# Kernel optimization log

Hardware: AMD Instinct MI355X
Metric: run time of the kernel (lower is better)

## Reference

```python
import jax, jax.numpy as jnp
import numpy as np
import math

D_MODEL = 512
N_HEADS = 8
D_HEAD = D_MODEL // N_HEADS
TEMP = math.sqrt(D_HEAD)


def setup_inputs() -> dict:
    key = jax.random.key(0)
    k1, k2, k3, k4, k5, k6 = jax.random.split(key, 6)
    B, L = 4, 2048
    q = jax.random.normal(k1, (B, L, D_MODEL), dtype=jnp.float32)
    # bool mask, True -> zero out post-softmax attention (matches torch.where branch)
    mask = jax.random.bernoulli(k2, 0.1, (B, L, L))
    in_weight = jax.random.normal(k3, (3 * D_MODEL, D_MODEL), dtype=jnp.float32) * 0.02
    in_bias = jax.random.normal(k4, (3 * D_MODEL,), dtype=jnp.float32) * 0.02
    out_w = jax.random.normal(k5, (D_MODEL, D_MODEL), dtype=jnp.float32) * 0.02
    out_b = jax.random.normal(k6, (D_MODEL,), dtype=jnp.float32) * 0.02
    return {"q": q, "mask": mask, "in_weight": in_weight, "in_bias": in_bias,
            "out_w": out_w, "out_b": out_b}


def reference(q, mask, in_weight, in_bias, out_w, out_b):
    B, L, D = q.shape
    # per-head weight slicing exactly as the torch reshape: (H, E, 3, D)
    W = in_weight.reshape(N_HEADS, D_HEAD, 3, D)
    Bv = in_bias.reshape(N_HEADS, D_HEAD, 3)
    qw, kw, vw = W[:, :, 0, :], W[:, :, 1, :], W[:, :, 2, :]  # (H, E, D)
    qb, kb, vb = Bv[:, :, 0], Bv[:, :, 1], Bv[:, :, 2]        # (H, E)
    # self-attention: k = q, v = q (forward defaults)
    Q = jnp.einsum('bld,hed->bhle', q, qw) + qb[None, :, None, :]
    K = jnp.einsum('bld,hed->bhle', q, kw) + kb[None, :, None, :]
    V = jnp.einsum('bld,hed->bhle', q, vw) + vb[None, :, None, :]
    atn = jax.nn.softmax(jnp.einsum('bhqe,bhke->bhqk', Q, K) / TEMP, axis=-1)
    # post-softmax bool masking (faithful to the original non-standard order)
    atn = jnp.where(mask[:, None, :, :], jnp.zeros((), atn.dtype), atn)
    # QUIRK of source: attention() returns V (not atn @ V); heads = concat of V
    heads = V.transpose(0, 2, 1, 3).reshape(B, L, D)  # (B, L, D_MODEL)
    outputs = heads @ out_w.T + out_b
    masks = atn.sum(axis=1)  # sum over heads -> (B, Lq, Lk)
    return outputs, masks
```

## Files before the change

kernel.cpp:

```cpp
#include <hip/hip_runtime.h>

typedef unsigned short u16;
typedef unsigned int u32;
typedef __bf16 bf16x8 __attribute__((ext_vector_type(8)));
typedef float f32x4 __attribute__((ext_vector_type(4)));

#define B_SZ 4
#define L_SZ 2048
#define D_SZ 512
#define H_SZ 8
#define E_SZ 64

#define Q_SCALE 0.18033688011112042f

#define WS_FLAG   0
#define WS_WPACK  1024
#define WS_BPACK  (WS_WPACK + 1572864)
#define WS_WOUT   (WS_BPACK + 6144)
#define WS_QBF    (WS_WOUT + 524288)
#define WS_Q      (WS_QBF + 8388608)
#define WS_K      (WS_Q + 8388608)
#define WS_V      (WS_K + 8388608)
#define WS_STATS  (WS_V + 8388608)

static __device__ __forceinline__ u16 f2bf(float f) {
  unsigned int u = __float_as_uint(f);
  u += 0x7FFFu + ((u >> 16) & 1u);
  return (u16)(u >> 16);
}

static __device__ __forceinline__ float fexp2(float x) {
  return __builtin_amdgcn_exp2f(x);
}

union FragU { bf16x8 v; uint4 u4; unsigned long long ul[2]; };

static __device__ __forceinline__ int gperm(int d) {
  int t = d & 31;
  return (d & ~31) | ((t & 12) << 1) | ((t & 16) >> 2) | (t & 3);
}

static __device__ __forceinline__ bf16x8 qfrag(const u16* __restrict__ Qp,
                                               int row, int half, int lg) {
  FragU f;
  f.u4 = *reinterpret_cast<const uint4*>(
      (const char*)Qp + (size_t)row * 128 + (half << 6) + (lg << 4));
  return f.v;
}

static __device__ __forceinline__ void gload_lds16(const void* g, void* l) {
  __builtin_amdgcn_global_load_lds(
      (const __attribute__((address_space(1))) void*)g,
      (__attribute__((address_space(3))) void*)l, 16, 0, 0);
}

template<int NT, int NCHUNK>
static __device__ __forceinline__ void stage_ktile(const u16* __restrict__ Kh, int kb0,
                                                   char* tile, int tid) {
  int wbase = (tid & ~63) * 16;
#pragma unroll
  for (int i = 0; i < NCHUNK / NT; i++) {
    int cl = tid + i * NT;
    int r = cl >> 3, c = cl & 7;
    const char* g = (const char*)Kh + (size_t)(kb0 + r) * 128 + ((c ^ (r & 7)) << 4);
    gload_lds16(g, tile + wbase + i * NT * 16);
  }
}

static __device__ __forceinline__ bf16x8 lds_frag(const char* tile, int c, int half,
                                                  int lr, int lg) {
  int r = c * 16 + lr;
  int off = ((half << 6) | (lg << 4)) ^ ((r & 7) << 4);
  FragU f;
  f.u4 = *reinterpret_cast<const uint4*>(tile + r * 128 + off);
  return f.v;
}

__global__ __launch_bounds__(256) void kdetect(const unsigned int* __restrict__ w,
                                               int* __restrict__ flag) {
  int fB = 0, fF = 0;
  for (int i = blockIdx.x * blockDim.x + threadIdx.x; i < 262144;
       i += gridDim.x * blockDim.x) {
    unsigned int v = w[i];
    if (v == 0x3F800000u) fF = 1;
    else if (v > 1u) fB = 1;
  }
  if (__any(fB)) { if ((threadIdx.x & 63) == 0) atomicOr(&flag[0], 1); }
  if (__any(fF)) { if ((threadIdx.x & 63) == 0) atomicOr(&flag[1], 1); }
}

__global__ __launch_bounds__(256) void kcast(const float* __restrict__ q,
                                             u16* __restrict__ qbf) {
  int i = blockIdx.x * blockDim.x + threadIdx.x;
  int row = i >> 6, c = i & 63;
  int g = c >> 2, lg = c & 3;
  const float* src = q + (size_t)row * 512 + g * 32 + lg * 4;
  float4 v0 = *reinterpret_cast<const float4*>(src);
  float4 v1 = *reinterpret_cast<const float4*>(src + 16);
  u32 w0 = f2bf(v0.x) | ((u32)f2bf(v0.y) << 16);
  u32 w1 = f2bf(v0.z) | ((u32)f2bf(v0.w) << 16);
  u32 w2 = f2bf(v1.x) | ((u32)f2bf(v1.y) << 16);
  u32 w3 = f2bf(v1.z) | ((u32)f2bf(v1.w) << 16);
  uint4 out = {w0, w1, w2, w3};
  *reinterpret_cast<uint4*>(qbf + (size_t)row * 512 + c * 8) = out;
}

__global__ __launch_bounds__(256) void kpack(const float* __restrict__ w_in,
                                             const float* __restrict__ b_in,
                                             const float* __restrict__ w_out,
                                             u16* __restrict__ Wpack, float* __restrict__ bpack,
                                             u16* __restrict__ Wout) {
  const int T0 = 1536 * 512;
  const int T1 = T0 + 512 * 512;
  const int T2 = T1 + 1536;
  for (int i = blockIdx.x * blockDim.x + threadIdx.x; i < T2; i += gridDim.x * blockDim.x) {
    if (i < T0) {
      int n = i >> 9, d = i & 511;
      int sel = n >> 9, idx = n & 511;
      int h = idx >> 6, e = idx & 63;
      int row = h * 192 + e * 3 + sel;
      float v = w_in[row * 512 + d];
      if (sel == 0) v *= Q_SCALE;
      Wpack[(size_t)n * 512 + gperm(d)] = f2bf(v);
    } else if (i < T1) {
      int j = i - T0;
      int n = j >> 9, d = j & 511;
      Wout[(size_t)n * 512 + gperm(d)] = f2bf(w_out[j]);
    } else {
      int n = i - T1;
      int sel = n >> 9, idx = n & 511;
      int h = idx >> 6, e = idx & 63;
      int row = h * 192 + e * 3 + sel;
      float v = b_in[row];
      if (sel == 0) v *= Q_SCALE;
      bpack[n] = v;
    }
  }
}

static __device__ __forceinline__ void stage_tile(const u16* __restrict__ A,
                                                  const u16* __restrict__ Bw,
                                                  int m0, int n0, int t,
                                                  char* tA, char* tB, int tid) {
  int w64 = tid & ~63;
#pragma unroll
  for (int i = 0; i < 4; i++) {
    int cl = tid + i * 256;
    int r = cl >> 3, c = cl & 7;
    size_t gofs = (size_t)r * 1024 + t * 128 + ((c ^ (r & 7)) << 4);
    gload_lds16((const char*)A + (size_t)m0 * 1024 + gofs, tA + (i * 256 + w64) * 16);
    gload_lds16((const char*)Bw + (size_t)n0 * 1024 + gofs, tB + (i * 256 + w64) * 16);
  }
}

template<int MODE>
__global__ __launch_bounds__(256) void kgemm(const u16* __restrict__ A,
                                             const u16* __restrict__ Bw,
                                             const float* __restrict__ bias,
                                             u16* __restrict__ Qb, u16* __restrict__ Kb,
                                             u16* __restrict__ Vb, float* __restrict__ outp) {
  __shared__ __align__(128) char tA[2][16384], tB[2][16384];
  int tid = threadIdx.x;
  int w = tid >> 6, lane = tid & 63;
  int lr = lane & 15, lg = lane >> 4;
  int m0 = blockIdx.x * 128, n0 = blockIdx.y * 128;
  int wr = w >> 1, wc = w & 1;

  f32x4 acc[4][4] = {};

  stage_tile(A, Bw, m0, n0, 0, tA[0], tB[0], tid);
  __syncthreads();
#pragma unroll 1
  for (int t = 0; t < 8; t++) {
    if (t < 7) stage_tile(A, Bw, m0, n0, t + 1, tA[(t + 1) & 1], tB[(t + 1) & 1], tid);
    const char* mA = tA[t & 1] + wr * 64 * 128;
    const char* mB = tB[t & 1] + wc * 64 * 128;
#pragma unroll
    for (int gg = 0; gg < 2; gg++) {
      bf16x8 af[4], bf_[4];
#pragma unroll
      for (int i = 0; i < 4; i++) af[i] = lds_frag(mA, i, gg, lr, lg);
#pragma unroll
      for (int j = 0; j < 4; j++) bf_[j] = lds_frag(mB, j, gg, lr, lg);
#pragma unroll
      for (int i = 0; i < 4; i++)
#pragma unroll
        for (int j = 0; j < 4; j++)
          acc[i][j] = __builtin_amdgcn_mfma_f32_16x16x32_bf16(af[i], bf_[j], acc[i][j], 0, 0, 0);
    }
    __syncthreads();
  }

#pragma unroll
  for (int j = 0; j < 4; j++) {
    int col = n0 + wc * 64 + j * 16 + lr;
    float bb = bias[col];
#pragma unroll
    for (int i = 0; i < 4; i++) {
#pragma unroll
      for (int jj = 0; jj < 4; jj++) {
        int row = m0 + wr * 64 + i * 16 + lg * 4 + jj;
        float val = acc[i][j][jj] + bb;
        if (MODE == 1) {
          outp[(size_t)row * 512 + col] = val;
        } else {
          u16 bv = f2bf(val);
          int b = row >> 11, l = row & 2047;
          if (col < 512) {
            int h = col >> 6, e = col & 63;
            Qb[((((size_t)(b * 8 + h)) << 11) + l) * 64 + gperm(e)] = bv;
          } else if (col < 1024) {
            int c2 = col - 512, h = c2 >> 6, e = c2 & 63;
            Kb[((((size_t)(b * 8 + h)) << 11) + l) * 64 + gperm(e)] = bv;
          } else {
            Vb[(size_t)row * 512 + gperm(col - 1024)] = bv;
          }
        }
      }
    }
  }
}

__global__ __launch_bounds__(256, 4) void kstats(const u16* __restrict__ Qb,
                                                 const u16* __restrict__ Kb,
                                                 float* __restrict__ stats) {
  __shared__ __align__(128) char tile[2][8192];
  int bh = blockIdx.x;
  int tid = threadIdx.x;
  int w = tid >> 6, lane = tid & 63;
  int lr = lane & 15, lg = lane >> 4;
  int q0 = blockIdx.y * 64 + w * 16;
  const u16* Qp = Qb + (size_t)bh * L_SZ * E_SZ;
  const u16* Kp = Kb + (size_t)bh * L_SZ * E_SZ;

  bf16x8 bq0 = qfrag(Qp, q0 + lr, 0, lg);
  bf16x8 bq1 = qfrag(Qp, q0 + lr, 1, lg);
  float s0 = 0.0f;

  stage_ktile<256, 512>(Kp, 0, tile[0], tid);
  __syncthreads();
#pragma unroll 1
  for (int t = 0; t < 32; t++) {
    if (t + 1 < 32) stage_ktile<256, 512>(Kp, (t + 1) * 64, tile[(t + 1) & 1], tid);
    const char* tl = tile[t & 1];
#pragma unroll
    for (int c = 0; c < 4; c++) {
      bf16x8 a0 = lds_frag(tl, c, 0, lr, lg);
      bf16x8 a1 = lds_frag(tl, c, 1, lr, lg);
      f32x4 d = {0.f, 0.f, 0.f, 0.f};
      d = __builtin_amdgcn_mfma_f32_16x16x32_bf16(a0, bq0, d, 0, 0, 0);
      d = __builtin_amdgcn_mfma_f32_16x16x32_bf16(a1, bq1, d, 0, 0, 0);
      s0 += fexp2(d[0]) + fexp2(d[1]) + fexp2(d[2]) + fexp2(d[3]);
    }
    __syncthreads();
  }
  s0 += __shfl_xor(s0, 16);
  s0 += __shfl_xor(s0, 32);
  if (lane < 16) stats[(size_t)bh * L_SZ + q0 + lr] = 1.0f / s0;
}

#define KM_PACKMASK(BITS, QOFS)                                                  \
  {                                                                              \
    size_t moff = mb + (size_t)(q0 + (QOFS) + lr) * L_SZ + kb0;                  \
    if (mode == 0) {                                                             \
      _Pragma("unroll")                                                          \
      for (int c = 0; c < 4; c++) {                                              \
        int4 mi = *reinterpret_cast<const int4*>((const int*)mask + moff + c * 16 + lg * 4); \
        BITS |= (mi.x ? 1u : 0u) << (c * 4);                                     \
        BITS |= (mi.y ? 1u : 0u) << (c * 4 + 1);                                 \
        BITS |= (mi.z ? 1u : 0u) << (c * 4 + 2);                                 \
        BITS |= (mi.w ? 1u : 0u) << (c * 4 + 3);                                 \
      }                                                                          \
    } else if (mode == 1) {                                                      \
      _Pragma("unroll")                                                          \
      for (int c = 0; c < 4; c++) {                                              \
        u32 mw = *reinterpret_cast<const u32*>((const unsigned char*)mask + moff + c * 16 + lg * 4); \
        BITS |= ((mw & 0x000000FFu) ? 1u : 0u) << (c * 4);                       \
        BITS |= ((mw & 0x0000FF00u) ? 1u : 0u) << (c * 4 + 1);                   \
        BITS |= ((mw & 0x00FF0000u) ? 1u : 0u) << (c * 4 + 2);                   \
        BITS |= ((mw & 0xFF000000u) ? 1u : 0u) << (c * 4 + 3);                   \
      }                                                                          \
    } else {                                                                     \
      _Pragma("unroll")                                                          \
      for (int c = 0; c < 4; c++) {                                              \
        float4 mf = *reinterpret_cast<const float4*>((const float*)mask + moff + c * 16 + lg * 4); \
        BITS |= ((mf.x != 0.f) ? 1u : 0u) << (c * 4);                            \
        BITS |= ((mf.y != 0.f) ? 1u : 0u) << (c * 4 + 1);                        \
        BITS |= ((mf.z != 0.f) ? 1u : 0u) << (c * 4 + 2);                        \
        BITS |= ((mf.w != 0.f) ? 1u : 0u) << (c * 4 + 3);                        \
      }                                                                          \
    }                                                                            \
  }

#define KM_EPILOGUE(PACC, QOFS, BITS)                                            \
  {                                                                              \
    int q = q0 + (QOFS) + lr;                                                    \
    float* mrow = mbase_out + (size_t)q * L_SZ + kb0;                            \
    _Pragma("unroll")                                                            \
    for (int c = 0; c < 4; c++) {                                                \
      int kk = c * 16 + lg * 4;                                                  \
      f32x4 v = PACC[c];                                                         \
      if ((BITS >> (c * 4 + 0)) & 1u) v[0] = 0.f;                                \
      if ((BITS >> (c * 4 + 1)) & 1u) v[1] = 0.f;                                \
      if ((BITS >> (c * 4 + 2)) & 1u) v[2] = 0.f;                                \
      if ((BITS >> (c * 4 + 3)) & 1u) v[3] = 0.f;                                \
      *reinterpret_cast<f32x4*>(mrow + kk) = v;                                  \
    }                                                                            \
  }

__global__ __launch_bounds__(256, 4) void kmasks(const u16* __restrict__ Qb,
                                                 const u16* __restrict__ Kb,
                                                 const float* __restrict__ stats,
                                                 const void* __restrict__ mask,
                                                 const int* __restrict__ flag,
                                                 float* __restrict__ outp) {
  __shared__ __align__(128) char tile[2][8192];
  int b = blockIdx.z;
  int tid = threadIdx.x;
  int w = tid >> 6, lane = tid & 63;
  int lr = lane & 15, lg = lane >> 4;
  int q0 = blockIdx.y * 128 + w * 32;
  int kb0 = blockIdx.x * 64;
  int mode = flag[0] ? 1 : (flag[1] ? 2 : 0);
  const size_t LE = (size_t)L_SZ * E_SZ;
  size_t mb = (size_t)b * L_SZ * L_SZ;

  f32x4 P0[4] = {}, P1[4] = {};

  stage_ktile<256, 512>(Kb + (size_t)(b * 8) * LE, kb0, tile[0], tid);
  const u16* Q0 = Qb + (size_t)(b * 8) * LE;
  bf16x8 nq0 = qfrag(Q0, q0 + lr, 0, lg);
  bf16x8 nq1 = qfrag(Q0, q0 + lr, 1, lg);
  bf16x8 nq2 = qfrag(Q0, q0 + 16 + lr, 0, lg);
  bf16x8 nq3 = qfrag(Q0, q0 + 16 + lr, 1, lg);
  float nr0 = stats[(size_t)(b * 8) * L_SZ + q0 + lr];
  float nr1 = stats[(size_t)(b * 8) * L_SZ + q0 + 16 + lr];
  u32 bits0 = 0, bits1 = 0;
  KM_PACKMASK(bits0, 0)
  KM_PACKMASK(bits1, 16)
  __syncthreads();

#pragma unroll 1
  for (int h = 0; h < 8; h++) {
    bf16x8 bq0 = nq0, bq1 = nq1, bq2 = nq2, bq3 = nq3;
    float rr0 = nr0, rr1 = nr1;
    if (h + 1 < 8) {
      stage_ktile<256, 512>(Kb + (size_t)(b * 8 + h + 1) * LE, kb0, tile[(h + 1) & 1], tid);
      const u16* Qn = Qb + (size_t)(b * 8 + h + 1) * LE;
      nq0 = qfrag(Qn, q0 + lr, 0, lg);
      nq1 = qfrag(Qn, q0 + lr, 1, lg);
      nq2 = qfrag(Qn, q0 + 16 + lr, 0, lg);
      nq3 = qfrag(Qn, q0 + 16 + lr, 1, lg);
      nr0 = stats[(size_t)(b * 8 + h + 1) * L_SZ + q0 + lr];
      nr1 = stats[(size_t)(b * 8 + h + 1) * L_SZ + q0 + 16 + lr];
    }
    const char* tl = tile[h & 1];
#pragma unroll
    for (int c = 0; c < 4; c++) {
      bf16x8 a0 = lds_frag(tl, c, 0, lr, lg);
      bf16x8 a1 = lds_frag(tl, c, 1, lr, lg);
      f32x4 d0 = {0.f, 0.f, 0.f, 0.f}, d1 = {0.f, 0.f, 0.f, 0.f};
      d0 = __builtin_amdgcn_mfma_f32_16x16x32_bf16(a0, bq0, d0, 0, 0, 0);
      d0 = __builtin_amdgcn_mfma_f32_16x16x32_bf16(a1, bq1, d0, 0, 0, 0);
      d1 = __builtin_amdgcn_mfma_f32_16x16x32_bf16(a0, bq2, d1, 0, 0, 0);
      d1 = __builtin_amdgcn_mfma_f32_16x16x32_bf16(a1, bq3, d1, 0, 0, 0);
#pragma unroll
      for (int j = 0; j < 4; j++) {
        P0[c][j] += fexp2(d0[j]) * rr0;
        P1[c][j] += fexp2(d1[j]) * rr1;
      }
    }
    __syncthreads();
  }

  float* mbase_out = outp + (size_t)B_SZ * L_SZ * D_SZ + (size_t)b * L_SZ * L_SZ;
  KM_EPILOGUE(P0, 0, bits0)
  KM_EPILOGUE(P1, 16, bits1)
}

extern "C" void kernel_launch(void* const* d_in, const int* in_sizes, int n_in,
                              void* d_out, int out_size, void* d_ws, size_t ws_size,
                              hipStream_t stream) {
  (void)in_sizes; (void)n_in; (void)out_size; (void)ws_size;
  const float* q     = (const float*)d_in[0];
  const void*  mask  = d_in[1];
  const float* w_in  = (const float*)d_in[2];
  const float* b_in  = (const float*)d_in[3];
  const float* w_out = (const float*)d_in[4];
  const float* b_out = (const float*)d_in[5];
  float* outp = (float*)d_out;
  char* ws = (char*)d_ws;

  int*    flag  = (int*)(ws + WS_FLAG);
  u16*    Wpack = (u16*)(ws + WS_WPACK);
  float*  bpack = (float*)(ws + WS_BPACK);
  u16*    Wout  = (u16*)(ws + WS_WOUT);
  u16*    qbf   = (u16*)(ws + WS_QBF);
  u16*    Qb    = (u16*)(ws + WS_Q);
  u16*    Kb    = (u16*)(ws + WS_K);
  u16*    Vb    = (u16*)(ws + WS_V);
  float*  stats = (float*)(ws + WS_STATS);

  hipMemsetAsync(flag, 0, 16, stream);
  hipLaunchKernelGGL(kdetect, dim3(256), dim3(256), 0, stream, (const unsigned int*)mask, flag);
  hipLaunchKernelGGL(kcast, dim3(2048), dim3(256), 0, stream, q, qbf);
  hipLaunchKernelGGL(kpack, dim3(2048), dim3(256), 0, stream, w_in, b_in, w_out,
                     Wpack, bpack, Wout);
  hipLaunchKernelGGL((kgemm<0>), dim3(64, 12), dim3(256), 0, stream,
                     qbf, Wpack, bpack, Qb, Kb, Vb, (float*)nullptr);
  hipLaunchKernelGGL((kgemm<1>), dim3(64, 4), dim3(256), 0, stream,
                     Vb, Wout, b_out, (u16*)nullptr, (u16*)nullptr, (u16*)nullptr, outp);
  hipLaunchKernelGGL(kstats, dim3(32, 32), dim3(256), 0, stream, Qb, Kb, stats);
  hipLaunchKernelGGL(kmasks, dim3(32, 16, 4), dim3(256), 0, stream, Qb, Kb, stats, mask, flag, outp);
}
```

Measured before the change: 139.2 us.

## Shrink kmasks tiles and preload all heads' K tiles in one LDS stage

The masks kernel now uses 64x32 output tiles per block (16 query rows per wave, 32 keys) instead of 128x64, which launches four times as many blocks. All eight heads' K tiles are loaded into LDS up front with direct global-to-LDS loads, and all heads' Q fragments and stats go into registers, so the per-head double-buffer loop and its barriers go away. The intent is more parallelism and fewer synchronisations in the kernel that writes the large probability output. In exchange, the 32KB LDS use and the larger register set may limit occupancy, and Q fragments and K tiles are reloaded more often across the smaller blocks.

```diff
diff --git a/kernel.cpp b/kernel.cpp
--- a/kernel.cpp
+++ b/kernel.cpp
@@ -264,7 +264,7 @@
     size_t moff = mb + (size_t)(q0 + (QOFS) + lr) * L_SZ + kb0;                  \
     if (mode == 0) {                                                             \
       _Pragma("unroll")                                                          \
-      for (int c = 0; c < 4; c++) {                                              \
+      for (int c = 0; c < 2; c++) {                                              \
         int4 mi = *reinterpret_cast<const int4*>((const int*)mask + moff + c * 16 + lg * 4); \
         BITS |= (mi.x ? 1u : 0u) << (c * 4);                                     \
         BITS |= (mi.y ? 1u : 0u) << (c * 4 + 1);                                 \
@@ -273,7 +273,7 @@
       }                                                                          \
     } else if (mode == 1) {                                                      \
       _Pragma("unroll")                                                          \
-      for (int c = 0; c < 4; c++) {                                              \
+      for (int c = 0; c < 2; c++) {                                              \
         u32 mw = *reinterpret_cast<const u32*>((const unsigned char*)mask + moff + c * 16 + lg * 4); \
         BITS |= ((mw & 0x000000FFu) ? 1u : 0u) << (c * 4);                       \
         BITS |= ((mw & 0x0000FF00u) ? 1u : 0u) << (c * 4 + 1);                   \
@@ -282,7 +282,7 @@
       }                                                                          \
     } else {                                                                     \
       _Pragma("unroll")                                                          \
-      for (int c = 0; c < 4; c++) {                                              \
+      for (int c = 0; c < 2; c++) {                                              \
         float4 mf = *reinterpret_cast<const float4*>((const float*)mask + moff + c * 16 + lg * 4); \
         BITS |= ((mf.x != 0.f) ? 1u : 0u) << (c * 4);                            \
         BITS |= ((mf.y != 0.f) ? 1u : 0u) << (c * 4 + 1);                        \
@@ -292,90 +292,92 @@
     }                                                                            \
   }
 
-#define KM_EPILOGUE(PACC, QOFS, BITS)                                            \
-  {                                                                              \
-    int q = q0 + (QOFS) + lr;                                                    \
-    float* mrow = mbase_out + (size_t)q * L_SZ + kb0;                            \
-    _Pragma("unroll")                                                            \
-    for (int c = 0; c < 4; c++) {                                                \
-      int kk = c * 16 + lg * 4;                                                  \
-      f32x4 v = PACC[c];                                                         \
-      if ((BITS >> (c * 4 + 0)) & 1u) v[0] = 0.f;                                \
-      if ((BITS >> (c * 4 + 1)) & 1u) v[1] = 0.f;                                \
-      if ((BITS >> (c * 4 + 2)) & 1u) v[2] = 0.f;                                \
-      if ((BITS >> (c * 4 + 3)) & 1u) v[3] = 0.f;                                \
-      *reinterpret_cast<f32x4*>(mrow + kk) = v;                                  \
-    }                                                                            \
-  }
-
 __global__ __launch_bounds__(256, 4) void kmasks(const u16* __restrict__ Qb,
                                                  const u16* __restrict__ Kb,
                                                  const float* __restrict__ stats,
                                                  const void* __restrict__ mask,
                                                  const int* __restrict__ flag,
                                                  float* __restrict__ outp) {
-  __shared__ __align__(128) char tile[2][8192];
+  __shared__ __align__(128) char tile[32768];
   int b = blockIdx.z;
   int tid = threadIdx.x;
-  int w = tid >> 6, lane = tid & 63;
+  int lane = tid & 63;
   int lr = lane & 15, lg = lane >> 4;
-  int q0 = blockIdx.y * 128 + w * 32;
-  int kb0 = blockIdx.x * 64;
+  int w = tid >> 6;
+  int q0 = blockIdx.y * 64 + w * 16;
+  int kb0 = blockIdx.x * 32;
   int mode = flag[0] ? 1 : (flag[1] ? 2 : 0);
   const size_t LE = (size_t)L_SZ * E_SZ;
   size_t mb = (size_t)b * L_SZ * L_SZ;
 
-  f32x4 P0[4] = {}, P1[4] = {};
-
-  stage_ktile<256, 512>(Kb + (size_t)(b * 8) * LE, kb0, tile[0], tid);
-  const u16* Q0 = Qb + (size_t)(b * 8) * LE;
-  bf16x8 nq0 = qfrag(Q0, q0 + lr, 0, lg);
-  bf16x8 nq1 = qfrag(Q0, q0 + lr, 1, lg);
-  bf16x8 nq2 = qfrag(Q0, q0 + 16 + lr, 0, lg);
-  bf16x8 nq3 = qfrag(Q0, q0 + 16 + lr, 1, lg);
-  float nr0 = stats[(size_t)(b * 8) * L_SZ + q0 + lr];
-  float nr1 = stats[(size_t)(b * 8) * L_SZ + q0 + 16 + lr];
-  u32 bits0 = 0, bits1 = 0;
+  {
+    int wbase = (tid & ~63) * 16;
+#pragma unroll
+    for (int i = 0; i < 8; i++) {
+      int r = tid >> 3, cc = tid & 7;
+      const char* g = (const char*)(Kb + (size_t)(b * 8 + i) * LE)
+                    + (size_t)(kb0 + r) * 128 + ((cc ^ (r & 7)) << 4);
+      gload_lds16(g, tile + (i * 256 + (tid & ~63)) * 16 + (wbase - (tid & ~63) * 16));
+    }
+  }
+
+  bf16x8 qh0[8], qh1[8];
+  float rr[8];
+#pragma unroll
+  for (int h = 0; h < 8; h++) {
+    const u16* Qp = Qb + (size_t)(b * 8 + h) * LE;
+    qh0[h] = qfrag(Qp, q0 + lr, 0, lg);
+    qh1[h] = qfrag(Qp, q0 + lr, 1, lg);
+    rr[h] = stats[(size_t)(b * 8 + h) * L_SZ + q0 + lr];
+  }
+
+  u32 bits0 = 0;
   KM_PACKMASK(bits0, 0)
-  KM_PACKMASK(bits1, 16)
+
   __syncthreads();
 
-#pragma unroll 1
+  f32x4 P0 = {0.f, 0.f, 0.f, 0.f}, P1 = {0.f, 0.f, 0.f, 0.f};
+#pragma unroll
   for (int h = 0; h < 8; h++) {
-    bf16x8 bq0 = nq0, bq1 = nq1, bq2 = nq2, bq3 = nq3;
-    float rr0 = nr0, rr1 = nr1;
-    if (h + 1 < 8) {
-      stage_ktile<256, 512>(Kb + (size_t)(b * 8 + h + 1) * LE, kb0, tile[(h + 1) & 1], tid);
-      const u16* Qn = Qb + (size_t)(b * 8 + h + 1) * LE;
-      nq0 = qfrag(Qn, q0 + lr, 0, lg);
-      nq1 = qfrag(Qn, q0 + lr, 1, lg);
-      nq2 = qfrag(Qn, q0 + 16 + lr, 0, lg);
-      nq3 = qfrag(Qn, q0 + 16 + lr, 1, lg);
-      nr0 = stats[(size_t)(b * 8 + h + 1) * L_SZ + q0 + lr];
-      nr1 = stats[(size_t)(b * 8 + h + 1) * L_SZ + q0 + 16 + lr];
-    }
-    const char* tl = tile[h & 1];
-#pragma unroll
-    for (int c = 0; c < 4; c++) {
-      bf16x8 a0 = lds_frag(tl, c, 0, lr, lg);
-      bf16x8 a1 = lds_frag(tl, c, 1, lr, lg);
-      f32x4 d0 = {0.f, 0.f, 0.f, 0.f}, d1 = {0.f, 0.f, 0.f, 0.f};
-      d0 = __builtin_amdgcn_mfma_f32_16x16x32_bf16(a0, bq0, d0, 0, 0, 0);
-      d0 = __builtin_amdgcn_mfma_f32_16x16x32_bf16(a1, bq1, d0, 0, 0, 0);
-      d1 = __builtin_amdgcn_mfma_f32_16x16x32_bf16(a0, bq2, d1, 0, 0, 0);
-      d1 = __builtin_amdgcn_mfma_f32_16x16x32_bf16(a1, bq3, d1, 0, 0, 0);
-#pragma unroll
-      for (int j = 0; j < 4; j++) {
-        P0[c][j] += fexp2(d0[j]) * rr0;
-        P1[c][j] += fexp2(d1[j]) * rr1;
-      }
-    }
-    __syncthreads();
-  }
-
-  float* mbase_out = outp + (size_t)B_SZ * L_SZ * D_SZ + (size_t)b * L_SZ * L_SZ;
-  KM_EPILOGUE(P0, 0, bits0)
-  KM_EPILOGUE(P1, 16, bits1)
+    const char* th = tile + h * 4096;
+    {
+      bf16x8 a0 = lds_frag(th, 0, 0, lr, lg);
+      bf16x8 a1 = lds_frag(th, 0, 1, lr, lg);
+      f32x4 d = {0.f, 0.f, 0.f, 0.f};
+      d = __builtin_amdgcn_mfma_f32_16x16x32_bf16(a0, qh0[h], d, 0, 0, 0);
+      d = __builtin_amdgcn_mfma_f32_16x16x32_bf16(a1, qh1[h], d, 0, 0, 0);
+#pragma unroll
+      for (int j = 0; j < 4; j++) P0[j] += fexp2(d[j]) * rr[h];
+    }
+    {
+      bf16x8 a0 = lds_frag(th, 1, 0, lr, lg);
+      bf16x8 a1 = lds_frag(th, 1, 1, lr, lg);
+      f32x4 d = {0.f, 0.f, 0.f, 0.f};
+      d = __builtin_amdgcn_mfma_f32_16x16x32_bf16(a0, qh0[h], d, 0, 0, 0);
+      d = __builtin_amdgcn_mfma_f32_16x16x32_bf16(a1, qh1[h], d, 0, 0, 0);
+#pragma unroll
+      for (int j = 0; j < 4; j++) P1[j] += fexp2(d[j]) * rr[h];
+    }
+  }
+
+  float* mrow = outp + (size_t)B_SZ * L_SZ * D_SZ + mb
+              + (size_t)(q0 + lr) * L_SZ + kb0;
+  {
+    f32x4 v = P0;
+    if ((bits0 >> 0) & 1u) v[0] = 0.f;
+    if ((bits0 >> 1) & 1u) v[1] = 0.f;
+    if ((bits0 >> 2) & 1u) v[2] = 0.f;
+    if ((bits0 >> 3) & 1u) v[3] = 0.f;
+    *reinterpret_cast<f32x4*>(mrow + lg * 4) = v;
+  }
+  {
+    f32x4 v = P1;
+    if ((bits0 >> 4) & 1u) v[0] = 0.f;
+    if ((bits0 >> 5) & 1u) v[1] = 0.f;
+    if ((bits0 >> 6) & 1u) v[2] = 0.f;
+    if ((bits0 >> 7) & 1u) v[3] = 0.f;
+    *reinterpret_cast<f32x4*>(mrow + 16 + lg * 4) = v;
+  }
 }
 
 extern "C" void kernel_launch(void* const* d_in, const int* in_sizes, int n_in,
@@ -411,5 +413,5 @@
   hipLaunchKernelGGL((kgemm<1>), dim3(64, 4), dim3(256), 0, stream,
                      Vb, Wout, b_out, (u16*)nullptr, (u16*)nullptr, (u16*)nullptr, outp);
   hipLaunchKernelGGL(kstats, dim3(32, 32), dim3(256), 0, stream, Qb, Kb, stats);
-  hipLaunchKernelGGL(kmasks, dim3(32, 16, 4), dim3(256), 0, stream, Qb, Kb, stats, mask, flag, outp);
-}
+  hipLaunchKernelGGL(kmasks, dim3(64, 32, 4), dim3(256), 0, stream, Qb, Kb, stats, mask, flag, outp);
+}
```

After: 168.0 us. +20.6%, slower.
